# Kernel tuning notes

Measured on AMD Instinct MI355X. Metric: run time of the kernel, lower is better.

The kernel has to match this reference:

```python
import jax, jax.numpy as jnp
import numpy as np

MUL = 128            # multiplicity of 0e and 1o node irreps
N_NODES = 10000
N_EDGES = 160000
R_BASIS = 8          # edge_feats_irreps.num_irreps
HIDDEN = 64
W_NUMEL = 4 * MUL    # conv_tp.weight_numel (4 uvu paths, edge mul = 1)
SQRT3 = 3.0 ** 0.5
SILU_2MOM = 1.679177   # e3nn normalize2mom constant for SiLU
AVG_NUM_NEIGHBORS = 10.0


def setup_inputs() -> dict:
    key = jax.random.key(0)
    ks = jax.random.split(key, 12)
    rn = lambda k, s: jax.random.normal(k, s, dtype=jnp.float32)
    return {
        "node_feats": rn(ks[0], (N_NODES, 4 * MUL)),        # 128x0e + 128x1o
        "edge_attrs": rn(ks[1], (N_EDGES, 4)),               # 1x0e + 1x1o spherical harmonics
        "edge_feats": rn(ks[2], (N_EDGES, R_BASIS)),         # 8x0e radial basis
        "edge_index": jax.random.randint(ks[3], (2, N_EDGES), 0, N_NODES),
        "W_up0": rn(ks[4], (MUL, MUL)),                      # linear_up, 0e block
        "W_up1": rn(ks[5], (MUL, MUL)),                      # linear_up, 1o block
        "W_mlp1": rn(ks[6], (R_BASIS, HIDDEN)),
        "W_mlp2": rn(ks[7], (HIDDEN, HIDDEN)),
        "W_mlp3": rn(ks[8], (HIDDEN, HIDDEN)),
        "W_mlp4": rn(ks[9], (HIDDEN, W_NUMEL)),
        "W_out0": rn(ks[10], (2 * MUL, MUL)),                # linear: 256x0e -> 128x0e
        "W_out1": rn(ks[11], (2 * MUL, MUL)),                # linear: 256x1o -> 128x1o
    }


def _lin_irreps(x0, x1, W0, W1):
    # equivariant o3.Linear: per-irrep channel mixing with 1/sqrt(fan_in)
    y0 = (x0 @ W0) / jnp.sqrt(jnp.float32(W0.shape[0]))
    y1 = jnp.einsum('num,uv->nvm', x1, W1) / jnp.sqrt(jnp.float32(W1.shape[0]))
    return y0, y1


def _forward(node_feats, edge_attrs, edge_feats, edge_index,
             W_up0, W_up1, W_mlp1, W_mlp2, W_mlp3, W_mlp4, W_out0, W_out1):
    num_nodes = node_feats.shape[0]
    sender, receiver = edge_index[0], edge_index[1]

    # split node feats into irrep blocks: [N,128] scalars, [N,128,3] vectors
    x0 = node_feats[:, :MUL]
    x1 = node_feats[:, MUL:].reshape(num_nodes, MUL, 3)
    x0, x1 = _lin_irreps(x0, x1, W_up0, W_up1)  # linear_up

    # radial MLP (e3nn FullyConnectedNet with normalized SiLU) -> per-edge TP weights
    h = edge_feats
    for W in (W_mlp1, W_mlp2, W_mlp3):
        h = SILU_2MOM * jax.nn.silu((h @ W) / jnp.sqrt(jnp.float32(W.shape[0])))
    tpw = (h @ W_mlp4) / jnp.sqrt(jnp.float32(W_mlp4.shape[0]))  # [E, 4*MUL]
    w1, w2, w3, w4 = jnp.split(tpw, 4, axis=-1)  # per-path [E, MUL]

    # gather sender features
    s0 = x0[sender]              # [E, MUL]
    s1 = x1[sender]              # [E, MUL, 3]
    y0 = edge_attrs[:, 0:1]      # [E, 1]  (0e sh)
    y1 = edge_attrs[:, 1:4]      # [E, 3]  (1o sh)

    # weighted uvu CG tensor product (component norm: alpha = sqrt(2l_out+1), w3j sum-sq = 1)
    p1 = w1 * s0 * y0                                    # 0e x 0e -> 0e  [E, MUL]
    p2 = (w2 * s0)[:, :, None] * y1[:, None, :]          # 0e x 1o -> 1o  [E, MUL, 3]
    p3 = w3[:, :, None] * s1 * y0[:, None, :]            # 1o x 0e -> 1o  [E, MUL, 3]
    p4 = w4 * jnp.einsum('eum,em->eu', s1, y1) / SQRT3   # 1o x 1o -> 0e  [E, MUL]

    # irreps_mid.simplify() = 256x0e + 256x1o
    m0 = jnp.concatenate([p1, p4], axis=-1)              # [E, 2*MUL]
    m1 = jnp.concatenate([p2, p3], axis=1)               # [E, 2*MUL, 3]

    # scatter-sum over receivers
    msg0 = jax.ops.segment_sum(m0, receiver, num_segments=num_nodes)
    msg1 = jax.ops.segment_sum(m1, receiver, num_segments=num_nodes)

    o0, o1 = _lin_irreps(msg0, msg1, W_out0, W_out1)
    out = jnp.concatenate([o0, o1.reshape(num_nodes, 3 * MUL)], axis=-1)
    return out / AVG_NUM_NEIGHBORS


def reference(node_feats, edge_attrs, edge_feats, edge_index,
              W_up0, W_up1, W_mlp1, W_mlp2, W_mlp3, W_mlp4, W_out0, W_out1):
    return _forward(node_feats, edge_attrs, edge_feats, edge_index,
                    W_up0, W_up1, W_mlp1, W_mlp2, W_mlp3, W_mlp4, W_out0, W_out1)
```

## Files before the change

### kernel.cpp

```cpp
#include <hip/hip_runtime.h>
#include <stdint.h>

#define NN 10000
#define NE 160000

typedef short short8 __attribute__((ext_vector_type(8)));
typedef float f32x4 __attribute__((ext_vector_type(4)));

__device__ __forceinline__ float bf2f(unsigned short u) {
    return __uint_as_float(((uint32_t)u) << 16);
}
__device__ __forceinline__ float bflo(uint32_t u) { return __uint_as_float(u << 16); }
__device__ __forceinline__ float bfhi(uint32_t u) { return __uint_as_float(u & 0xffff0000u); }
__device__ __forceinline__ unsigned short f2bf(float f) {
    uint32_t u = __float_as_uint(f);
    u += 0x7fffu + ((u >> 16) & 1u);
    return (unsigned short)(u >> 16);
}
__device__ __forceinline__ uint32_t pack2(float lo, float hi) {
    return (uint32_t)f2bf(lo) | ((uint32_t)f2bf(hi) << 16);
}
__device__ __forceinline__ float silu2(float x) {
    return 1.679177f * x / (1.f + __expf(-x));
}

__global__ __launch_bounds__(256) void k_wup(const float* __restrict__ Wu0,
                                             const float* __restrict__ Wu1,
                                             unsigned short* __restrict__ w0T,
                                             unsigned short* __restrict__ w1T) {
    const float s = 0.08838834764831845f;
    for (int i = threadIdx.x + blockIdx.x * 256; i < 16384; i += 256 * 64) {
        int u = i >> 7, v = i & 127;
        w0T[v * 128 + u] = f2bf(Wu0[i] * s);
        w1T[v * 128 + u] = f2bf(Wu1[i] * s);
    }
}

__global__ __launch_bounds__(256) void k_prep(const float* __restrict__ nf,
                                              unsigned short* __restrict__ x0b,
                                              unsigned short* __restrict__ x1b) {
    int idx = blockIdx.x * 256 + threadIdx.x;
    int n = idx >> 7, u = idx & 127;
    const float* row = nf + (size_t)n * 512;
    x0b[(size_t)n * 128 + u] = f2bf(row[u]);
    const float* p = row + 128 + u * 3;
    x1b[(size_t)n * 128 + u]                = f2bf(p[0]);
    x1b[1280000 + (size_t)n * 128 + u]      = f2bf(p[1]);
    x1b[2560000 + (size_t)n * 128 + u]      = f2bf(p[2]);
}

__global__ __launch_bounds__(256) void k_upg(const unsigned short* __restrict__ x0b,
                                             const unsigned short* __restrict__ x1b,
                                             const unsigned short* __restrict__ w0T,
                                             const unsigned short* __restrict__ w1T,
                                             float* __restrict__ xw) {
    int wave = threadIdx.x >> 6, lane = threadIdx.x & 63;
    int wid = blockIdx.x * 4 + wave;
    if (wid >= 1250) return;
    int tile = wid >> 1, half = wid & 1;
    int n0 = tile * 16;
    int lm = lane & 15, lq = lane >> 4;

    uint4 A0[4], A1[3][4];
    const unsigned short* a0r = x0b + (size_t)(n0 + lm) * 128 + lq * 8;
#pragma unroll
    for (int kf = 0; kf < 4; ++kf) A0[kf] = *(const uint4*)(a0r + kf * 32);
#pragma unroll
    for (int m = 0; m < 3; ++m) {
        const unsigned short* a1r = x1b + 1280000 * (size_t)m + (size_t)(n0 + lm) * 128 + lq * 8;
#pragma unroll
        for (int kf = 0; kf < 4; ++kf) A1[m][kf] = *(const uint4*)(a1r + kf * 32);
    }

    for (int vq = 0; vq < 4; ++vq) {
        int vt = half * 4 + vq;
        const unsigned short* b0r = w0T + (vt * 16 + lm) * 128 + lq * 8;
        const unsigned short* b1r = w1T + (vt * 16 + lm) * 128 + lq * 8;
        f32x4 acc0 = {0.f, 0.f, 0.f, 0.f};
#pragma unroll
        for (int kf = 0; kf < 4; ++kf) {
            short8 b = __builtin_bit_cast(short8, *(const uint4*)(b0r + kf * 32));
            acc0 = __builtin_amdgcn_mfma_f32_16x16x32_bf16(
                __builtin_bit_cast(short8, A0[kf]), b, acc0, 0, 0, 0);
        }
        f32x4 acc1[3];
#pragma unroll
        for (int m = 0; m < 3; ++m) acc1[m] = (f32x4){0.f, 0.f, 0.f, 0.f};
#pragma unroll
        for (int kf = 0; kf < 4; ++kf) {
            short8 b = __builtin_bit_cast(short8, *(const uint4*)(b1r + kf * 32));
#pragma unroll
            for (int m = 0; m < 3; ++m)
                acc1[m] = __builtin_amdgcn_mfma_f32_16x16x32_bf16(
                    __builtin_bit_cast(short8, A1[m][kf]), b, acc1[m], 0, 0, 0);
        }
        int col = vt * 16 + lm;
#pragma unroll
        for (int r = 0; r < 4; ++r) {
            float* o = xw + (size_t)(n0 + lq * 4 + r) * 512;
            o[col] = acc0[r];
            o[128 + col] = acc1[0][r];
            o[256 + col] = acc1[1][r];
            o[384 + col] = acc1[2][r];
        }
    }
}

__global__ __launch_bounds__(256) void k_wmlp(const float* __restrict__ W1,
                                              const float* __restrict__ W2,
                                              const float* __restrict__ W3,
                                              unsigned short* __restrict__ w1Tp,
                                              unsigned short* __restrict__ w2T,
                                              unsigned short* __restrict__ w3T) {
    int t = threadIdx.x;
    for (int i = t; i < 2048; i += 256) {
        int jj = i >> 5, k = i & 31;
        w1Tp[i] = (k < 8) ? f2bf(W1[k * 64 + jj] * 0.3535533905932738f) : 0;
    }
    for (int i = t; i < 4096; i += 256) {
        int jj = i >> 6, k = i & 63;
        w2T[i] = f2bf(W2[k * 64 + jj] * 0.125f);
        w3T[i] = f2bf(W3[k * 64 + jj] * 0.125f);
    }
}

__global__ __launch_bounds__(256) void k_mlp(const float* __restrict__ ef,
                                             const unsigned short* __restrict__ w1Tp,
                                             const unsigned short* __restrict__ w2T,
                                             const unsigned short* __restrict__ w3T,
                                             unsigned short* __restrict__ h3w) {
    __shared__ __align__(16) unsigned short hs_all[4][16 * 72];
    int wave = threadIdx.x >> 6, lane = threadIdx.x & 63;
    int lm = lane & 15, lq = lane >> 4;
    int e0 = blockIdx.x * 64 + wave * 16;
    unsigned short* h = hs_all[wave];
    unsigned short* hrow = h + lm * 72;

    uint4 A1[4];
#pragma unroll
    for (int mt = 0; mt < 4; ++mt)
        A1[mt] = *(const uint4*)(w1Tp + (mt * 16 + lm) * 32 + lq * 8);
    uint4 b = {0, 0, 0, 0};
    if (lq == 0) {
        const float4* p = (const float4*)(ef + (size_t)(e0 + lm) * 8);
        float4 x = p[0], y = p[1];
        b.x = pack2(x.x, x.y); b.y = pack2(x.z, x.w);
        b.z = pack2(y.x, y.y); b.w = pack2(y.z, y.w);
    }
    short8 bb = __builtin_bit_cast(short8, b);
#pragma unroll
    for (int mt = 0; mt < 4; ++mt) {
        f32x4 acc = {0.f, 0.f, 0.f, 0.f};
        acc = __builtin_amdgcn_mfma_f32_16x16x32_bf16(
            __builtin_bit_cast(short8, A1[mt]), bb, acc, 0, 0, 0);
        uint2 v;
        v.x = pack2(silu2(acc[0]), silu2(acc[1]));
        v.y = pack2(silu2(acc[2]), silu2(acc[3]));
        *(uint2*)(hrow + mt * 16 + lq * 4) = v;
    }

    uint4 A2[4][2];
#pragma unroll
    for (int mt = 0; mt < 4; ++mt)
#pragma unroll
        for (int kf = 0; kf < 2; ++kf)
            A2[mt][kf] = *(const uint4*)(w2T + (mt * 16 + lm) * 64 + kf * 32 + lq * 8);
    {
        short8 B0 = __builtin_bit_cast(short8, *(const uint4*)(hrow + lq * 8));
        short8 B1 = __builtin_bit_cast(short8, *(const uint4*)(hrow + 32 + lq * 8));
#pragma unroll
        for (int mt = 0; mt < 4; ++mt) {
            f32x4 acc = {0.f, 0.f, 0.f, 0.f};
            acc = __builtin_amdgcn_mfma_f32_16x16x32_bf16(
                __builtin_bit_cast(short8, A2[mt][0]), B0, acc, 0, 0, 0);
            acc = __builtin_amdgcn_mfma_f32_16x16x32_bf16(
                __builtin_bit_cast(short8, A2[mt][1]), B1, acc, 0, 0, 0);
            uint2 v;
            v.x = pack2(silu2(acc[0]), silu2(acc[1]));
            v.y = pack2(silu2(acc[2]), silu2(acc[3]));
            *(uint2*)(hrow + mt * 16 + lq * 4) = v;
        }
    }

    uint4 A3[4][2];
#pragma unroll
    for (int mt = 0; mt < 4; ++mt)
#pragma unroll
        for (int kf = 0; kf < 2; ++kf)
            A3[mt][kf] = *(const uint4*)(w3T + (mt * 16 + lm) * 64 + kf * 32 + lq * 8);
    {
        short8 B0 = __builtin_bit_cast(short8, *(const uint4*)(hrow + lq * 8));
        short8 B1 = __builtin_bit_cast(short8, *(const uint4*)(hrow + 32 + lq * 8));
#pragma unroll
        for (int mt = 0; mt < 4; ++mt) {
            f32x4 acc = {0.f, 0.f, 0.f, 0.f};
            acc = __builtin_amdgcn_mfma_f32_16x16x32_bf16(
                __builtin_bit_cast(short8, A3[mt][0]), B0, acc, 0, 0, 0);
            acc = __builtin_amdgcn_mfma_f32_16x16x32_bf16(
                __builtin_bit_cast(short8, A3[mt][1]), B1, acc, 0, 0, 0);
            uint2 v;
            v.x = pack2(silu2(acc[0]), silu2(acc[1]));
            v.y = pack2(silu2(acc[2]), silu2(acc[3]));
            *(uint2*)(hrow + mt * 16 + lq * 4) = v;
        }
    }

#pragma unroll
    for (int q = 0; q < 2; ++q) {
        int c = lane + q * 64;
        int row = c >> 3, col = (c & 7) * 8;
        *(uint4*)(h3w + (size_t)(e0 + row) * 64 + col) =
            *(const uint4*)(h + row * 72 + col);
    }
}

__global__ void k_zero(int* __restrict__ p, int n) {
    int i = blockIdx.x * 256 + threadIdx.x;
    if (i < n) p[i] = 0;
}
__global__ void k_hist(const int* __restrict__ ei, int* __restrict__ counts) {
    int e = blockIdx.x * 256 + threadIdx.x;
    if (e < NE) atomicAdd(&counts[ei[NE + e]], 1);
}
__global__ __launch_bounds__(1024) void k_scan(const int* __restrict__ counts,
                                               int* __restrict__ offs,
                                               int* __restrict__ cursor) {
    __shared__ int sums[1024];
    int t = threadIdx.x;
    int base = t * 10;
    int s = 0;
    for (int i = 0; i < 10; ++i) {
        int idx = base + i;
        if (idx < NN) s += counts[idx];
    }
    sums[t] = s;
    __syncthreads();
    for (int d = 1; d < 1024; d <<= 1) {
        int v = (t >= d) ? sums[t - d] : 0;
        __syncthreads();
        if (t >= d) sums[t] += v;
        __syncthreads();
    }
    int run = (t == 0) ? 0 : sums[t - 1];
    for (int i = 0; i < 10; ++i) {
        int idx = base + i;
        if (idx < NN) {
            offs[idx] = run;
            cursor[idx] = run;
            run += counts[idx];
        }
    }
    if (t == 0) offs[NN] = NE;
}
__global__ void k_fill(const int* __restrict__ ei, int* __restrict__ cursor,
                       int* __restrict__ elist) {
    int e = blockIdx.x * 256 + threadIdx.x;
    if (e < NE) {
        int slot = atomicAdd(&cursor[ei[NE + e]], 1);
        elist[slot] = e;
    }
}
__global__ void k_gather(const int* __restrict__ ei, const float* __restrict__ ea,
                         const int* __restrict__ elist,
                         int* __restrict__ eis, float4* __restrict__ eap) {
    int i = blockIdx.x * 256 + threadIdx.x;
    if (i < NE) {
        int e = elist[i];
        eis[i] = ei[e];
        eap[i] = *(const float4*)(ea + (size_t)e * 4);
    }
}

__global__ void k_w4t(const float* __restrict__ W4, unsigned short* __restrict__ w4T) {
    int idx = blockIdx.x * 256 + threadIdx.x;
    int k = idx >> 9, c = idx & 511;
    w4T[c * 64 + k] = f2bf(W4[idx]);
}
__global__ void k_wt2(const float* __restrict__ Wo0, const float* __restrict__ Wo1,
                      unsigned short* __restrict__ woT0, unsigned short* __restrict__ woT1) {
    int idx = blockIdx.x * 256 + threadIdx.x;
    int u = idx >> 7, v = idx & 127;
    woT0[v * 256 + u] = f2bf(Wo0[idx]);
    woT1[v * 256 + u] = f2bf(Wo1[idx]);
}

__global__ __launch_bounds__(256) void k_msg2(const float* __restrict__ xw,
                                              const unsigned short* __restrict__ h3w,
                                              const unsigned short* __restrict__ w4T,
                                              const int* __restrict__ eis,
                                              const float4* __restrict__ eap,
                                              const int* __restrict__ offs,
                                              const int* __restrict__ elist,
                                              unsigned short* __restrict__ msgb) {
    __shared__ __align__(16) float wl_all[4][16][132];
    int n = blockIdx.x, t = threadIdx.x;
    int j = t >> 6, lw = t & 63;
    int lm = lw & 15, lq = lw >> 4;
    int c0 = lw * 2;
    int beg = offs[n], end = offs[n + 1];
    float (*wl)[132] = wl_all[j];
    float a0 = 0.f, a1 = 0.f, a2 = 0.f, a3 = 0.f, a4 = 0.f, a5 = 0.f;

    if (end > beg) {
        const int last = end - 1;
        uint4 A[8][2];
        const unsigned short* aw = w4T + (size_t)(j * 8 * 16 + lm) * 64 + lq * 8;
#pragma unroll
        for (int mt = 0; mt < 8; ++mt)
#pragma unroll
            for (int kf = 0; kf < 2; ++kf)
                A[mt][kf] = *(const uint4*)(aw + mt * 1024 + kf * 32);

        for (int cbeg = beg; cbeg < end; cbeg += 16) {
            int slot = cbeg + lm;
            slot = slot <= last ? slot : last;
            int esrc = elist[slot];
            const unsigned short* hr = h3w + (size_t)esrc * 64 + lq * 8;
            short8 B0 = __builtin_bit_cast(short8, *(const uint4*)(hr));
            short8 B1 = __builtin_bit_cast(short8, *(const uint4*)(hr + 32));
#pragma unroll
            for (int mt = 0; mt < 8; ++mt) {
                f32x4 acc = {0.f, 0.f, 0.f, 0.f};
                acc = __builtin_amdgcn_mfma_f32_16x16x32_bf16(
                    __builtin_bit_cast(short8, A[mt][0]), B0, acc, 0, 0, 0);
                acc = __builtin_amdgcn_mfma_f32_16x16x32_bf16(
                    __builtin_bit_cast(short8, A[mt][1]), B1, acc, 0, 0, 0);
                acc = acc * 0.125f;
                *(f32x4*)&wl[lm][mt * 16 + lq * 4] = acc;
            }

            int cend = cbeg + 16 < end ? cbeg + 16 : end;
            if (j == 0) {
                for (int g = cbeg; g < cend; g += 8) {
                    int s_[8]; float wa[8], wb[8], ey[8]; float2 x[8];
#pragma unroll
                    for (int k = 0; k < 8; ++k) {
                        int idx = g + k;
                        int cl = idx <= last ? idx : last;
                        s_[k] = eis[cl];
                    }
#pragma unroll
                    for (int k = 0; k < 8; ++k) {
                        int idx = g + k;
                        int cl = idx <= last ? idx : last;
                        int e = idx - cbeg;
                        float2 wv = *(const float2*)&wl[e][c0];
                        wa[k] = idx <= last ? wv.x : 0.f;
                        wb[k] = idx <= last ? wv.y : 0.f;
                        ey[k] = eap[cl].x;
                        x[k] = *(const float2*)(xw + (size_t)s_[k] * 512 + c0);
                    }
#pragma unroll
                    for (int k = 0; k < 8; ++k) {
                        a0 += wa[k] * x[k].x * ey[k];
                        a1 += wb[k] * x[k].y * ey[k];
                    }
                }
            } else if (j == 1) {
                for (int g = cbeg; g < cend; g += 8) {
                    int s_[8]; float wa[8], wb[8], ex[8], ey[8], ez[8]; float2 x[8];
#pragma unroll
                    for (int k = 0; k < 8; ++k) {
                        int idx = g + k;
                        int cl = idx <= last ? idx : last;
                        s_[k] = eis[cl];
                    }
#pragma unroll
                    for (int k = 0; k < 8; ++k) {
                        int idx = g + k;
                        int cl = idx <= last ? idx : last;
                        int e = idx - cbeg;
                        float2 wv = *(const float2*)&wl[e][c0];
                        wa[k] = idx <= last ? wv.x : 0.f;
                        wb[k] = idx <= last ? wv.y : 0.f;
                        float4 ev = eap[cl];
                        ex[k] = ev.y; ey[k] = ev.z; ez[k] = ev.w;
                        x[k] = *(const float2*)(xw + (size_t)s_[k] * 512 + c0);
                    }
#pragma unroll
                    for (int k = 0; k < 8; ++k) {
                        float ta = wa[k] * x[k].x, tb = wb[k] * x[k].y;
                        a0 += ta * ex[k]; a1 += ta * ey[k]; a2 += ta * ez[k];
                        a3 += tb * ex[k]; a4 += tb * ey[k]; a5 += tb * ez[k];
                    }
                }
            } else if (j == 2) {
                for (int g = cbeg; g < cend; g += 8) {
                    int s_[8]; float wa[8], wb[8], ey[8];
                    float2 x0[8], x1[8], x2[8];
#pragma unroll
                    for (int k = 0; k < 8; ++k) {
                        int idx = g + k;
                        int cl = idx <= last ? idx : last;
                        s_[k] = eis[cl];
                    }
#pragma unroll
                    for (int k = 0; k < 8; ++k) {
                        int idx = g + k;
                        int cl = idx <= last ? idx : last;
                        int e = idx - cbeg;
                        float2 wv = *(const float2*)&wl[e][c0];
                        wa[k] = idx <= last ? wv.x : 0.f;
                        wb[k] = idx <= last ? wv.y : 0.f;
                        ey[k] = eap[cl].x;
                        const float* xr = xw + (size_t)s_[k] * 512 + c0;
                        x0[k] = *(const float2*)(xr + 128);
                        x1[k] = *(const float2*)(xr + 256);
                        x2[k] = *(const float2*)(xr + 384);
                    }
#pragma unroll
                    for (int k = 0; k < 8; ++k) {
                        float f0 = wa[k] * ey[k], f1 = wb[k] * ey[k];
                        a0 += f0 * x0[k].x; a1 += f0 * x1[k].x; a2 += f0 * x2[k].x;
                        a3 += f1 * x0[k].y; a4 += f1 * x1[k].y; a5 += f1 * x2[k].y;
                    }
                }
            } else {
                for (int g = cbeg; g < cend; g += 8) {
                    int s_[8]; float wa[8], wb[8], ex[8], ey[8], ez[8];
                    float2 x0[8], x1[8], x2[8];
#pragma unroll
                    for (int k = 0; k < 8; ++k) {
                        int idx = g + k;
                        int cl = idx <= last ? idx : last;
                        s_[k] = eis[cl];
                    }
#pragma unroll
                    for (int k = 0; k < 8; ++k) {
                        int idx = g + k;
                        int cl = idx <= last ? idx : last;
                        int e = idx - cbeg;
                        float2 wv = *(const float2*)&wl[e][c0];
                        wa[k] = idx <= last ? wv.x : 0.f;
                        wb[k] = idx <= last ? wv.y : 0.f;
                        float4 ev = eap[cl];
                        ex[k] = ev.y; ey[k] = ev.z; ez[k] = ev.w;
                        const float* xr = xw + (size_t)s_[k] * 512 + c0;
                        x0[k] = *(const float2*)(xr + 128);
                        x1[k] = *(const float2*)(xr + 256);
                        x2[k] = *(const float2*)(xr + 384);
                    }
#pragma unroll
                    for (int k = 0; k < 8; ++k) {
                        float dta = x0[k].x * ex[k] + x1[k].x * ey[k] + x2[k].x * ez[k];
                        float dtb = x0[k].y * ex[k] + x1[k].y * ey[k] + x2[k].y * ez[k];
                        a0 += wa[k] * dta * 0.5773502691896258f;
                        a1 += wb[k] * dtb * 0.5773502691896258f;
                    }
                }
            }
        }
    }

    unsigned short* mr = msgb + (size_t)n * 1024;
    if (j == 0) {
        *(uint32_t*)(mr + c0) = pack2(a0, a1);
    } else if (j == 1) {
        *(uint32_t*)(mr + 256 + c0)       = pack2(a0, a3);
        *(uint32_t*)(mr + 256 + 256 + c0) = pack2(a1, a4);
        *(uint32_t*)(mr + 256 + 512 + c0) = pack2(a2, a5);
    } else if (j == 2) {
        *(uint32_t*)(mr + 256 + 128 + c0)       = pack2(a0, a3);
        *(uint32_t*)(mr + 256 + 256 + 128 + c0) = pack2(a1, a4);
        *(uint32_t*)(mr + 256 + 512 + 128 + c0) = pack2(a2, a5);
    } else {
        *(uint32_t*)(mr + 128 + c0) = pack2(a0, a1);
    }
}

__global__ __launch_bounds__(256) void k_out0(const unsigned short* __restrict__ msgb,
                                              const unsigned short* __restrict__ woT,
                                              float* __restrict__ out) {
    int wave = threadIdx.x >> 6, lane = threadIdx.x & 63;
    int wid = blockIdx.x * 4 + wave;
    if (wid >= NN / 16) return;
    int n0 = wid * 16;
    int lm = lane & 15, lq = lane >> 4;
    uint4 A[8];
    const unsigned short* ar = msgb + (size_t)(n0 + lm) * 1024 + lq * 8;
#pragma unroll
    for (int kf = 0; kf < 8; ++kf) A[kf] = *(const uint4*)(ar + kf * 32);
    const unsigned short* br = woT + lm * 256 + lq * 8;
    float* ob = out + (size_t)n0 * 512;
    for (int vt = 0; vt < 8; ++vt) {
        f32x4 acc = {0.f, 0.f, 0.f, 0.f};
#pragma unroll
        for (int kf = 0; kf < 8; ++kf) {
            uint4 b = *(const uint4*)(br + vt * 16 * 256 + kf * 32);
            acc = __builtin_amdgcn_mfma_f32_16x16x32_bf16(
                __builtin_bit_cast(short8, A[kf]), __builtin_bit_cast(short8, b), acc, 0, 0, 0);
        }
#pragma unroll
        for (int r = 0; r < 4; ++r)
            ob[(size_t)(lq * 4 + r) * 512 + vt * 16 + lm] = acc[r] * 0.00625f;
    }
}

__global__ __launch_bounds__(256) void k_out1(const unsigned short* __restrict__ msgb,
                                              const unsigned short* __restrict__ woT,
                                              float* __restrict__ out) {
    int wave = threadIdx.x >> 6, lane = threadIdx.x & 63;
    int wid = blockIdx.x * 4 + wave;
    if (wid >= NN / 16) return;
    int n0 = wid * 16;
    int lm = lane & 15, lq = lane >> 4;
    uint4 A[3][8];
    const unsigned short* ar = msgb + (size_t)(n0 + lm) * 1024 + 256 + lq * 8;
#pragma unroll
    for (int m = 0; m < 3; ++m)
#pragma unroll
        for (int kf = 0; kf < 8; ++kf)
            A[m][kf] = *(const uint4*)(ar + m * 256 + kf * 32);
    const unsigned short* br = woT + lm * 256 + lq * 8;
    float* ob = out + (size_t)n0 * 512 + 128;
    for (int vt = 0; vt < 8; ++vt) {
        f32x4 acc[3];
#pragma unroll
        for (int m = 0; m < 3; ++m) acc[m] = (f32x4){0.f, 0.f, 0.f, 0.f};
#pragma unroll
        for (int kf = 0; kf < 8; ++kf) {
            uint4 braw = *(const uint4*)(br + vt * 16 * 256 + kf * 32);
            short8 b = __builtin_bit_cast(short8, braw);
#pragma unroll
            for (int m = 0; m < 3; ++m)
                acc[m] = __builtin_amdgcn_mfma_f32_16x16x32_bf16(
                    __builtin_bit_cast(short8, A[m][kf]), b, acc[m], 0, 0, 0);
        }
        int vb = (vt * 16 + lm) * 3;
#pragma unroll
        for (int r = 0; r < 4; ++r) {
            float* o = ob + (size_t)(lq * 4 + r) * 512 + vb;
            o[0] = acc[0][r] * 0.00625f;
            o[1] = acc[1][r] * 0.00625f;
            o[2] = acc[2][r] * 0.00625f;
        }
    }
}

extern "C" void kernel_launch(void* const* d_in, const int* in_sizes, int n_in,
                              void* d_out, int out_size, void* d_ws, size_t ws_size,
                              hipStream_t stream) {
    const float* nf  = (const float*)d_in[0];
    const float* ea  = (const float*)d_in[1];
    const float* ef  = (const float*)d_in[2];
    const int*   ei  = (const int*)d_in[3];
    const float* Wu0 = (const float*)d_in[4];
    const float* Wu1 = (const float*)d_in[5];
    const float* W1  = (const float*)d_in[6];
    const float* W2  = (const float*)d_in[7];
    const float* W3  = (const float*)d_in[8];
    const float* W4  = (const float*)d_in[9];
    const float* Wo0 = (const float*)d_in[10];
    const float* Wo1 = (const float*)d_in[11];
    float* out = (float*)d_out;
    char* ws = (char*)d_ws;

    unsigned short* x0b  = (unsigned short*)ws;
    unsigned short* x1b  = (unsigned short*)(ws + 2560000);
    unsigned short* woT0 = (unsigned short*)ws;
    unsigned short* woT1 = (unsigned short*)(ws + 65536);
    float4*         eap  = (float4*)(ws + 131072);
    int*            eis  = (int*)(ws + 131072 + 2560000);
    float*          xw   = (float*)(ws + 163840000);
    unsigned short* h3w  = (unsigned short*)(ws + 184320000);
    unsigned short* msgb = (unsigned short*)(ws + 204800000);
    unsigned short* w4T  = (unsigned short*)(ws + 225280000);
    int* ib     = (int*)(ws + 225280000 + 65536);
    int* counts = ib;
    int* offs   = ib + 10240;
    int* cursor = ib + 20480;
    int* elist  = ib + 30720;
    unsigned short* w1Tp = (unsigned short*)(ws + 226108416);
    unsigned short* w2T  = (unsigned short*)(ws + 226108416 + 4096);
    unsigned short* w3T  = (unsigned short*)(ws + 226108416 + 12288);
    unsigned short* w0T  = (unsigned short*)(ws + 226128896);
    unsigned short* w1T  = (unsigned short*)(ws + 226161664);

    k_wmlp <<<1, 256, 0, stream>>>(W1, W2, W3, w1Tp, w2T, w3T);
    k_wup  <<<64, 256, 0, stream>>>(Wu0, Wu1, w0T, w1T);
    k_prep <<<5000, 256, 0, stream>>>(nf, x0b, x1b);
    k_upg  <<<313, 256, 0, stream>>>(x0b, x1b, w0T, w1T, xw);
    k_mlp  <<<2500, 256, 0, stream>>>(ef, w1Tp, w2T, w3T, h3w);
    k_w4t  <<<128, 256, 0, stream>>>(W4, w4T);
    k_zero <<<40, 256, 0, stream>>>(counts, NN);
    k_hist <<<625, 256, 0, stream>>>(ei, counts);
    k_scan <<<1, 1024, 0, stream>>>(counts, offs, cursor);
    k_fill <<<625, 256, 0, stream>>>(ei, cursor, elist);
    k_wt2  <<<128, 256, 0, stream>>>(Wo0, Wo1, woT0, woT1);
    k_gather<<<625, 256, 0, stream>>>(ei, ea, elist, eis, eap);
    k_msg2 <<<NN, 256, 0, stream>>>(xw, h3w, w4T, eis, eap, offs, elist, msgb);
    k_out0 <<<157, 256, 0, stream>>>(msgb, woT0, out);
    k_out1 <<<157, 256, 0, stream>>>(msgb, woT1, out);
}
```

Before: 356.7 us.

## Split message kernel into one-wave blocks per path with bf16 LDS weights

The per-node message kernel now launches four 64-thread blocks per node, one per tensor-product path, instead of one 256-thread block with four waves. The A-fragment registers that were preloaded from w4T are dropped and reloaded from global or cache inside each MFMA iteration, and the per-edge weight staging in shared memory is stored as bf16 instead of fp32. The aim is to cut register and LDS pressure and let waves schedule independently for higher occupancy. In exchange, each block redoes offsets and edge-index loads, w4T is reloaded repeatedly, and the edge weights lose precision by rounding to bf16.

Result: slower. 429.7 us (+20.5%).

```diff
diff --git a/kernel.cpp b/kernel.cpp
--- a/kernel.cpp
+++ b/kernel.cpp
@@ -284,32 +284,26 @@
     woT1[v * 256 + u] = f2bf(Wo1[idx]);
 }
 
-__global__ __launch_bounds__(256) void k_msg2(const float* __restrict__ xw,
-                                              const unsigned short* __restrict__ h3w,
-                                              const unsigned short* __restrict__ w4T,
-                                              const int* __restrict__ eis,
-                                              const float4* __restrict__ eap,
-                                              const int* __restrict__ offs,
-                                              const int* __restrict__ elist,
-                                              unsigned short* __restrict__ msgb) {
-    __shared__ __align__(16) float wl_all[4][16][132];
-    int n = blockIdx.x, t = threadIdx.x;
-    int j = t >> 6, lw = t & 63;
+__global__ __launch_bounds__(64, 4) void k_msg2(const float* __restrict__ xw,
+                                                const unsigned short* __restrict__ h3w,
+                                                const unsigned short* __restrict__ w4T,
+                                                const int* __restrict__ eis,
+                                                const float4* __restrict__ eap,
+                                                const int* __restrict__ offs,
+                                                const int* __restrict__ elist,
+                                                unsigned short* __restrict__ msgb) {
+    __shared__ __align__(8) unsigned short wl[16][130];
+    int bid = blockIdx.x;
+    int n = bid >> 2, j = bid & 3;
+    int lw = threadIdx.x;
     int lm = lw & 15, lq = lw >> 4;
     int c0 = lw * 2;
     int beg = offs[n], end = offs[n + 1];
-    float (*wl)[132] = wl_all[j];
     float a0 = 0.f, a1 = 0.f, a2 = 0.f, a3 = 0.f, a4 = 0.f, a5 = 0.f;
 
     if (end > beg) {
         const int last = end - 1;
-        uint4 A[8][2];
-        const unsigned short* aw = w4T + (size_t)(j * 8 * 16 + lm) * 64 + lq * 8;
-#pragma unroll
-        for (int mt = 0; mt < 8; ++mt)
-#pragma unroll
-            for (int kf = 0; kf < 2; ++kf)
-                A[mt][kf] = *(const uint4*)(aw + mt * 1024 + kf * 32);
+        const unsigned short* aw = w4T + (size_t)(j * 128 + lm) * 64 + lq * 8;
 
         for (int cbeg = beg; cbeg < end; cbeg += 16) {
             int slot = cbeg + lm;
@@ -320,13 +314,17 @@
             short8 B1 = __builtin_bit_cast(short8, *(const uint4*)(hr + 32));
 #pragma unroll
             for (int mt = 0; mt < 8; ++mt) {
+                uint4 a0r = *(const uint4*)(aw + mt * 1024);
+                uint4 a1r = *(const uint4*)(aw + mt * 1024 + 32);
                 f32x4 acc = {0.f, 0.f, 0.f, 0.f};
                 acc = __builtin_amdgcn_mfma_f32_16x16x32_bf16(
-                    __builtin_bit_cast(short8, A[mt][0]), B0, acc, 0, 0, 0);
+                    __builtin_bit_cast(short8, a0r), B0, acc, 0, 0, 0);
                 acc = __builtin_amdgcn_mfma_f32_16x16x32_bf16(
-                    __builtin_bit_cast(short8, A[mt][1]), B1, acc, 0, 0, 0);
-                acc = acc * 0.125f;
-                *(f32x4*)&wl[lm][mt * 16 + lq * 4] = acc;
+                    __builtin_bit_cast(short8, a1r), B1, acc, 0, 0, 0);
+                uint2 v;
+                v.x = pack2(acc[0] * 0.125f, acc[1] * 0.125f);
+                v.y = pack2(acc[2] * 0.125f, acc[3] * 0.125f);
+                *(uint2*)&wl[lm][mt * 16 + lq * 4] = v;
             }
 
             int cend = cbeg + 16 < end ? cbeg + 16 : end;
@@ -344,9 +342,9 @@
                         int idx = g + k;
                         int cl = idx <= last ? idx : last;
                         int e = idx - cbeg;
-                        float2 wv = *(const float2*)&wl[e][c0];
-                        wa[k] = idx <= last ? wv.x : 0.f;
-                        wb[k] = idx <= last ? wv.y : 0.f;
+                        uint32_t w = *(const uint32_t*)&wl[e][c0];
+                        wa[k] = idx <= last ? bflo(w) : 0.f;
+                        wb[k] = idx <= last ? bfhi(w) : 0.f;
                         ey[k] = eap[cl].x;
                         x[k] = *(const float2*)(xw + (size_t)s_[k] * 512 + c0);
                     }
@@ -370,9 +368,9 @@
                         int idx = g + k;
                         int cl = idx <= last ? idx : last;
                         int e = idx - cbeg;
-                        float2 wv = *(const float2*)&wl[e][c0];
-                        wa[k] = idx <= last ? wv.x : 0.f;
-                        wb[k] = idx <= last ? wv.y : 0.f;
+                        uint32_t w = *(const uint32_t*)&wl[e][c0];
+                        wa[k] = idx <= last ? bflo(w) : 0.f;
+                        wb[k] = idx <= last ? bfhi(w) : 0.f;
                         float4 ev = eap[cl];
                         ex[k] = ev.y; ey[k] = ev.z; ez[k] = ev.w;
                         x[k] = *(const float2*)(xw + (size_t)s_[k] * 512 + c0);
@@ -399,9 +397,9 @@
                         int idx = g + k;
                         int cl = idx <= last ? idx : last;
                         int e = idx - cbeg;
-                        float2 wv = *(const float2*)&wl[e][c0];
-                        wa[k] = idx <= last ? wv.x : 0.f;
-                        wb[k] = idx <= last ? wv.y : 0.f;
+                        uint32_t w = *(const uint32_t*)&wl[e][c0];
+                        wa[k] = idx <= last ? bflo(w) : 0.f;
+                        wb[k] = idx <= last ? bfhi(w) : 0.f;
                         ey[k] = eap[cl].x;
                         const float* xr = xw + (size_t)s_[k] * 512 + c0;
                         x0[k] = *(const float2*)(xr + 128);
@@ -430,9 +428,9 @@
                         int idx = g + k;
                         int cl = idx <= last ? idx : last;
                         int e = idx - cbeg;
-                        float2 wv = *(const float2*)&wl[e][c0];
-                        wa[k] = idx <= last ? wv.x : 0.f;
-                        wb[k] = idx <= last ? wv.y : 0.f;
+                        uint32_t w = *(const uint32_t*)&wl[e][c0];
+                        wa[k] = idx <= last ? bflo(w) : 0.f;
+                        wb[k] = idx <= last ? bfhi(w) : 0.f;
                         float4 ev = eap[cl];
                         ex[k] = ev.y; ey[k] = ev.z; ez[k] = ev.w;
                         const float* xr = xw + (size_t)s_[k] * 512 + c0;
@@ -588,7 +586,7 @@
     k_fill <<<625, 256, 0, stream>>>(ei, cursor, elist);
     k_wt2  <<<128, 256, 0, stream>>>(Wo0, Wo1, woT0, woT1);
     k_gather<<<625, 256, 0, stream>>>(ei, ea, elist, eis, eap);
-    k_msg2 <<<NN, 256, 0, stream>>>(xw, h3w, w4T, eis, eap, offs, elist, msgb);
+    k_msg2 <<<NN * 4, 64, 0, stream>>>(xw, h3w, w4T, eis, eap, offs, elist, msgb);
     k_out0 <<<157, 256, 0, stream>>>(msgb, woT0, out);
     k_out1 <<<157, 256, 0, stream>>>(msgb, woT1, out);
 }
```
